# Kernel optimization log

Hardware: AMD Instinct MI355X
Metric: run time of the kernel (lower is better)

## Reference

```python
import jax, jax.numpy as jnp
import numpy as np

D_MODEL, D_INNER, D_STATE, DT_RANK, K = 768, 1536, 16, 48, 4
B, L = 2, 1024


def causal_depthwise_conv(x, w, b):
    # x: [B, L, D], w: [D, 1, K], b: [D]; torch pads K-1 both sides then slices [:L] -> causal left pad
    xt = x.transpose(0, 2, 1)  # [B, D, L]
    out = jax.lax.conv_general_dilated(
        xt, w, window_strides=(1,), padding=[(K - 1, 0)],
        dimension_numbers=('NCH', 'OIH', 'NCH'), feature_group_count=xt.shape[1])
    return out.transpose(0, 2, 1) + b


def ssm(xc, A_log, D, W_dt, dtW, dtb, W_B, W_C):
    # xc: [B, L, Din]
    A = -jnp.exp(A_log)                                   # [Din, N]
    dt_low = jnp.einsum('bld,rd->blr', xc, W_dt)          # [B, L, R]
    delta = jax.nn.softplus(jnp.einsum('blr,dr->bld', dt_low, dtW) + dtb)  # [B, L, Din]
    Bm = jnp.einsum('bld,nd->bln', xc, W_B)               # [B, L, N]
    Cm = jnp.einsum('bld,nd->bln', xc, W_C)               # [B, L, N]
    deltaA = jnp.exp(delta[..., None] * A)                # [B, L, Din, N]
    BX = (delta * xc)[..., None] * Bm[:, :, None, :]      # [B, L, Din, N]

    def combine(e1, e2):
        a1, b1 = e1
        a2, b2 = e2
        return a1 * a2, a2 * b1 + b2

    _, hs = jax.lax.associative_scan(combine, (deltaA, BX), axis=1)  # [B, L, Din, N]
    y = jnp.einsum('bldn,bln->bld', hs, Cm) + D * xc
    return y


def setup_inputs() -> dict:
    key = jax.random.key(0)
    ks = jax.random.split(key, 20)
    s = 0.02
    A_init = jnp.log(jnp.broadcast_to(jnp.arange(1, D_STATE + 1, dtype=jnp.float32), (D_INNER, D_STATE)))
    return {
        'x': jax.random.normal(ks[0], (B, L, D_MODEL), jnp.float32),
        'W_in_states': jax.random.normal(ks[1], (D_INNER, D_MODEL), jnp.float32) * s,
        'W_in_gates': jax.random.normal(ks[2], (D_INNER, D_MODEL), jnp.float32) * s,
        'conv_w': jax.random.normal(ks[3], (D_INNER, 1, K), jnp.float32) * 0.2,
        'conv_b': jax.random.normal(ks[4], (D_INNER,), jnp.float32) * 0.02,
        'conv_w_b': jax.random.normal(ks[5], (D_INNER, 1, K), jnp.float32) * 0.2,
        'conv_b_b': jax.random.normal(ks[6], (D_INNER,), jnp.float32) * 0.02,
        'W_dt': jax.random.normal(ks[7], (DT_RANK, D_INNER), jnp.float32) * s,
        'W_B': jax.random.normal(ks[8], (D_STATE, D_INNER), jnp.float32) * s,
        'W_C': jax.random.normal(ks[9], (D_STATE, D_INNER), jnp.float32) * s,
        'dtW': jax.random.normal(ks[10], (D_INNER, DT_RANK), jnp.float32) * s,
        'dtb': jax.random.normal(ks[11], (D_INNER,), jnp.float32) * 0.1,
        'A_log': A_init,
        'Dp': jnp.ones((D_INNER,), jnp.float32),
        'W_dt_b': jax.random.normal(ks[12], (DT_RANK, D_INNER), jnp.float32) * s,
        'W_B_b': jax.random.normal(ks[13], (D_STATE, D_INNER), jnp.float32) * s,
        'W_C_b': jax.random.normal(ks[14], (D_STATE, D_INNER), jnp.float32) * s,
        'dtW_b': jax.random.normal(ks[15], (D_INNER, DT_RANK), jnp.float32) * s,
        'dtb_b': jax.random.normal(ks[16], (D_INNER,), jnp.float32) * 0.1,
        'A_log_b': A_init,
        'Dp_b': jnp.ones((D_INNER,), jnp.float32),
        'W_out': jax.random.normal(ks[17], (D_MODEL, D_INNER), jnp.float32) * s,
    }


def reference(x, W_in_states, W_in_gates, conv_w, conv_b, conv_w_b, conv_b_b,
              W_dt, W_B, W_C, dtW, dtb, A_log, Dp,
              W_dt_b, W_B_b, W_C_b, dtW_b, dtb_b, A_log_b, Dp_b, W_out):
    xs = jnp.einsum('blm,dm->bld', x, W_in_states)  # [B, L, Din]
    z = jnp.einsum('blm,dm->bld', x, W_in_gates)    # [B, L, Din]
    # forward branch
    xc = jax.nn.silu(causal_depthwise_conv(xs, conv_w, conv_b))
    y = ssm(xc, A_log, Dp, W_dt, dtW, dtb, W_B, W_C)
    # backward branch: xz flipped along L, split -> reversed xs / reversed z
    xs_b = xs[:, ::-1]
    z_b = z[:, ::-1]
    xcb = jax.nn.silu(causal_depthwise_conv(xs_b, conv_w_b, conv_b_b))
    y_b = ssm(xcb, A_log_b, Dp_b, W_dt_b, dtW_b, dtb_b, W_B_b, W_C_b)
    # gating
    y = y * jax.nn.silu(z)
    y_b = y_b * jax.nn.silu(z_b)
    y = (y + y_b[:, ::-1]) * 0.5  # divide_output
    return jnp.einsum('bld,md->blm', y, W_out)
```

## Files before the change

### kernel.cpp

```cpp
#include <hip/hip_runtime.h>
#include <hip/hip_bf16.h>
#include <stdint.h>

#define DM 768
#define DI 1536
#define DSTATE 16
#define RNK 48
#define BB 2
#define LL 1024
#define ML (BB * LL)

#define NSEG 32
#define SEGL (LL / NSEG)

typedef unsigned short u16;
typedef __bf16 bf16x8 __attribute__((ext_vector_type(8)));
typedef float f32x4 __attribute__((ext_vector_type(4)));

struct __align__(8) u16x4_t { u16 x, y, z, w; };

__device__ __forceinline__ float b2f(u16 u) {
  union { uint32_t i; float f; } v; v.i = ((uint32_t)u) << 16; return v.f;
}
__device__ __forceinline__ u16 f2b(float f) {
  union { float f; uint32_t i; } v; v.f = f;
  uint32_t r = v.i + 0x7FFFu + ((v.i >> 16) & 1u);
  return (u16)(r >> 16);
}
__device__ __forceinline__ float silu_f(float x) { return x / (1.f + __expf(-x)); }
__device__ __forceinline__ float softplus_f(float s) {
  return fmaxf(s, 0.f) + __logf(1.f + __expf(-fabsf(s)));
}
__device__ __forceinline__ u16x4_t cvt4(float4 v) {
  u16x4_t o; o.x = f2b(v.x); o.y = f2b(v.y); o.z = f2b(v.z); o.w = f2b(v.w); return o;
}

#define SEG_X    (ML * DM / 4)
#define SEG_W    (DI * DM / 4)
#define SEG_CAT  (128 * DI / 4)
#define SEG_DTW  (DI * 64 / 4)
__global__ __launch_bounds__(256) void convert_kernel(
    const float4* __restrict__ x, const float4* __restrict__ wis,
    const float4* __restrict__ wig, const float4* __restrict__ wout,
    const float* __restrict__ W_B, const float* __restrict__ W_C,
    const float* __restrict__ W_dt,
    const float* __restrict__ W_B_b, const float* __restrict__ W_C_b,
    const float* __restrict__ W_dt_b,
    const float* __restrict__ dtW, const float* __restrict__ dtW_b,
    u16x4_t* __restrict__ xb, u16x4_t* __restrict__ wisb,
    u16x4_t* __restrict__ wigb, u16x4_t* __restrict__ woutb,
    u16x4_t* __restrict__ wcf, u16x4_t* __restrict__ wcb,
    u16x4_t* __restrict__ dtwf, u16x4_t* __restrict__ dtwb)
{
  int idx = blockIdx.x * 256 + threadIdx.x;
  if (idx < SEG_X) { xb[idx] = cvt4(x[idx]); return; }
  idx -= SEG_X;
  if (idx < SEG_W) { wisb[idx] = cvt4(wis[idx]); return; }
  idx -= SEG_W;
  if (idx < SEG_W) { wigb[idx] = cvt4(wig[idx]); return; }
  idx -= SEG_W;
  if (idx < SEG_W) { woutb[idx] = cvt4(wout[idx]); return; }
  idx -= SEG_W;
  if (idx < 2 * SEG_CAT) {
    int dir = idx / SEG_CAT;
    int rem = idx % SEG_CAT;
    int row = rem / (DI / 4), k4 = rem % (DI / 4);
    const float* src = nullptr;
    if (row < 16)      src = (dir ? W_B_b  : W_B)  + (size_t)row * DI + k4 * 4;
    else if (row < 32) src = (dir ? W_C_b  : W_C)  + (size_t)(row - 16) * DI + k4 * 4;
    else if (row < 80) src = (dir ? W_dt_b : W_dt) + (size_t)(row - 32) * DI + k4 * 4;
    u16x4_t o;
    if (src) o = cvt4(*(const float4*)src);
    else { o.x = 0; o.y = 0; o.z = 0; o.w = 0; }
    (dir ? wcb : wcf)[rem] = o;
    return;
  }
  idx -= 2 * SEG_CAT;
  int dir = idx / SEG_DTW;
  int rem = idx % SEG_DTW;
  int d = rem / 16, r4 = rem % 16;
  const float* Dw = dir ? dtW_b : dtW;
  u16x4_t o;
  if (r4 < 12) o = cvt4(*(const float4*)(Dw + (size_t)d * RNK + r4 * 4));
  else { o.x = 0; o.y = 0; o.z = 0; o.w = 0; }
  (dir ? dtwb : dtwf)[rem] = o;
}

__global__ __launch_bounds__(256) void gemm_bt(
    const u16* __restrict__ A, const u16* __restrict__ B0,
    const u16* __restrict__ B1, int Nsplit,
    void* __restrict__ Cout, int M, int N, int K, int ldc, int epi,
    const u16* __restrict__ A2, const u16* __restrict__ B2,
    void* __restrict__ C2,
    u16* __restrict__ Caux, u16* __restrict__ Caux2,
    const float* __restrict__ ebias, const float* __restrict__ ebias2)
{
  if (blockIdx.z) { A = A2; B0 = B2; Cout = C2; Caux = Caux2; ebias = ebias2; }
  __shared__ alignas(16) u16 As[128 * 32];
  __shared__ alignas(16) u16 Bs[128 * 32];
  const int tid = threadIdx.x;
  const int wave = tid >> 6, lane = tid & 63;
  const int bm = blockIdx.y * 128;
  const int bn = blockIdx.x * 128;

  const u16* Bmat = B0;
  int ncol0 = bn;
  int epi_l = epi;
  if (B1 != nullptr && bn >= Nsplit) { Bmat = B1; ncol0 = bn - Nsplit; epi_l = 1; }

  const int c0 = tid, c1 = tid + 256;
  const u16* gA0 = A + (size_t)(bm + (c0 >> 2)) * K + (c0 & 3) * 8;
  const u16* gA1 = A + (size_t)(bm + (c1 >> 2)) * K + (c1 & 3) * 8;
  const u16* gB0 = Bmat + (size_t)(ncol0 + (c0 >> 2)) * K + (c0 & 3) * 8;
  const u16* gB1 = Bmat + (size_t)(ncol0 + (c1 >> 2)) * K + (c1 & 3) * 8;
  uint4* lA0 = (uint4*)&As[c0 * 8]; uint4* lA1 = (uint4*)&As[c1 * 8];
  uint4* lB0 = (uint4*)&Bs[c0 * 8]; uint4* lB1 = (uint4*)&Bs[c1 * 8];

  const int wm = (wave & 1) * 64, wn = (wave >> 1) * 64;
  const int rl = lane & 15, q = lane >> 4;

  f32x4 acc[4][4];
#pragma unroll
  for (int i = 0; i < 4; ++i)
#pragma unroll
    for (int j = 0; j < 4; ++j) acc[i][j] = (f32x4){0.f, 0.f, 0.f, 0.f};

  const bf16x8* AsV = (const bf16x8*)As;
  const bf16x8* BsV = (const bf16x8*)Bs;

  uint4 ra0 = *(const uint4*)(gA0);
  uint4 ra1 = *(const uint4*)(gA1);
  uint4 rb0 = *(const uint4*)(gB0);
  uint4 rb1 = *(const uint4*)(gB1);

  for (int k0 = 0; k0 < K; k0 += 32) {
    *lA0 = ra0; *lA1 = ra1; *lB0 = rb0; *lB1 = rb1;
    __syncthreads();
    if (k0 + 32 < K) {
      ra0 = *(const uint4*)(gA0 + k0 + 32);
      ra1 = *(const uint4*)(gA1 + k0 + 32);
      rb0 = *(const uint4*)(gB0 + k0 + 32);
      rb1 = *(const uint4*)(gB1 + k0 + 32);
    }
    bf16x8 af[4], bfv[4];
#pragma unroll
    for (int s = 0; s < 4; ++s) {
      af[s]  = AsV[(wm + s * 16 + rl) * 4 + q];
      bfv[s] = BsV[(wn + s * 16 + rl) * 4 + q];
    }
#pragma unroll
    for (int i = 0; i < 4; ++i)
#pragma unroll
      for (int j = 0; j < 4; ++j)
        acc[i][j] = __builtin_amdgcn_mfma_f32_16x16x32_bf16(af[i], bfv[j], acc[i][j], 0, 0, 0);
    __syncthreads();
  }

#pragma unroll
  for (int i = 0; i < 4; ++i) {
#pragma unroll
    for (int j = 0; j < 4; ++j) {
#pragma unroll
      for (int r = 0; r < 4; ++r) {
        int row = bm + wm + i * 16 + q * 4 + r;
        int col = bn + wn + j * 16 + rl;
        float v = acc[i][j][r];
        if (epi_l == 1) v = silu_f(v);
        if (epi == 5) {
          if (col < 32)      ((float*)Cout)[(size_t)row * 32 + col] = v;
          else if (col < 96) Caux[(size_t)row * 64 + (col - 32)] = f2b(v);
        } else if (epi == 6) {
          ((u16*)Cout)[(size_t)row * ldc + col] = f2b(softplus_f(v + ebias[col]));
        } else if (epi == 2) {
          ((float*)Cout)[(size_t)row * ldc + col] = v;
        } else {
          ((u16*)Cout)[(size_t)row * ldc + col] = f2b(v);
        }
      }
    }
  }
}

__global__ __launch_bounds__(256) void gemm_out64(
    const u16* __restrict__ A, const u16* __restrict__ Bw,
    float* __restrict__ out)
{
  __shared__ alignas(16) u16 As[64 * 72];
  __shared__ alignas(16) u16 Bs[64 * 72];
  const int tid = threadIdx.x;
  const int wave = tid >> 6, lane = tid & 63;
  const int bm = blockIdx.y * 64;
  const int bn = blockIdx.x * 64;

  const int c0 = tid, c1 = tid + 256;
  const u16* gA0 = A + (size_t)(bm + (c0 >> 3)) * DI + (c0 & 7) * 8;
  const u16* gA1 = A + (size_t)(bm + (c1 >> 3)) * DI + (c1 & 7) * 8;
  const u16* gB0 = Bw + (size_t)(bn + (c0 >> 3)) * DI + (c0 & 7) * 8;
  const u16* gB1 = Bw + (size_t)(bn + (c1 >> 3)) * DI + (c1 & 7) * 8;
  uint4* lA0 = (uint4*)&As[(c0 >> 3) * 72 + (c0 & 7) * 8];
  uint4* lA1 = (uint4*)&As[(c1 >> 3) * 72 + (c1 & 7) * 8];
  uint4* lB0 = (uint4*)&Bs[(c0 >> 3) * 72 + (c0 & 7) * 8];
  uint4* lB1 = (uint4*)&Bs[(c1 >> 3) * 72 + (c1 & 7) * 8];

  const int rl = lane & 15, q = lane >> 4;

  f32x4 acc[4];
#pragma unroll
  for (int s = 0; s < 4; ++s) acc[s] = (f32x4){0.f, 0.f, 0.f, 0.f};

  uint4 ra0 = *(const uint4*)gA0, ra1 = *(const uint4*)gA1;
  uint4 rb0 = *(const uint4*)gB0, rb1 = *(const uint4*)gB1;

  for (int k0 = 0; k0 < DI; k0 += 64) {
    *lA0 = ra0; *lA1 = ra1; *lB0 = rb0; *lB1 = rb1;
    __syncthreads();
    if (k0 + 64 < DI) {
      ra0 = *(const uint4*)(gA0 + k0 + 64);
      ra1 = *(const uint4*)(gA1 + k0 + 64);
      rb0 = *(const uint4*)(gB0 + k0 + 64);
      rb1 = *(const uint4*)(gB1 + k0 + 64);
    }
    bf16x8 bf[2], af;
#pragma unroll
    for (int c = 0; c < 2; ++c)
      bf[c] = *(const bf16x8*)&Bs[(wave * 16 + rl) * 72 + c * 32 + q * 8];
#pragma unroll
    for (int s = 0; s < 4; ++s) {
#pragma unroll
      for (int c = 0; c < 2; ++c) {
        af = *(const bf16x8*)&As[(s * 16 + rl) * 72 + c * 32 + q * 8];
        acc[s] = __builtin_amdgcn_mfma_f32_16x16x32_bf16(af, bf[c], acc[s], 0, 0, 0);
      }
    }
    __syncthreads();
  }

#pragma unroll
  for (int s = 0; s < 4; ++s) {
#pragma unroll
    for (int r = 0; r < 4; ++r) {
      int row = bm + s * 16 + q * 4 + r;
      int col = bn + wave * 16 + rl;
      out[(size_t)row * DM + col] = acc[s][r];
    }
  }
}

__global__ void conv_kernel(
    const u16* __restrict__ xsg,
    const float* __restrict__ cw, const float* __restrict__ cb,
    const float* __restrict__ cwb, const float* __restrict__ cbb,
    u16* __restrict__ xc, u16* __restrict__ xcb)
{
  int idx = blockIdx.x * 256 + threadIdx.x;
  int d = idx % DI;
  int row = idx / DI;
  int l = row % LL, b = row / LL;
  const u16* base = xsg + (size_t)b * LL * 3072 + d;

  float4 wf = *(const float4*)(cw + d * 4);
  float4 wb = *(const float4*)(cwb + d * 4);
  float wfk[4] = {wf.x, wf.y, wf.z, wf.w};
  float wbk[4] = {wb.x, wb.y, wb.z, wb.w};

  float accf = cb[d];
  float accb = cbb[d];
#pragma unroll
  for (int k = 0; k < 4; ++k) {
    int ls = l - 3 + k;
    if (ls >= 0) {
      accf += wfk[k] * b2f(base[(size_t)ls * 3072]);
      accb += wbk[k] * b2f(base[(size_t)(LL - 1 - ls) * 3072]);
    }
  }
  xc[idx]  = f2b(silu_f(accf));
  xcb[idx] = f2b(silu_f(accb));
}

__global__ void combine_kernel(
    const u16* __restrict__ ybr, const u16* __restrict__ xsg, u16* yf)
{
  int idx = blockIdx.x * 256 + threadIdx.x;
  int d = idx % DI;
  int row = idx / DI;
  int l = row % LL, b = row / LL;
  float g = b2f(xsg[(size_t)row * 3072 + DI + d]);
  float vb = b2f(ybr[((size_t)b * LL + (LL - 1 - l)) * DI + d]);
  float v = 0.5f * (b2f(yf[idx]) + vb) * g;
  yf[idx] = f2b(v);
}

__global__ __launch_bounds__(256) void scan_sum(
    const u16* __restrict__ df, const u16* __restrict__ db,
    const u16* __restrict__ xcf, const u16* __restrict__ xcb,
    const float* __restrict__ pf, const float* __restrict__ pb,
    const float* __restrict__ A_log, const float* __restrict__ A_log_b,
    float* __restrict__ sdl, float* __restrict__ bs)
{
  const int dir = blockIdx.z / NSEG, seg = blockIdx.z % NSEG;
  const u16* delta = dir ? db : df;
  const u16* xc = dir ? xcb : xcf;
  const float* proj = dir ? pb : pf;
  const float* Al = dir ? A_log_b : A_log;
  const int b = blockIdx.y;
  const int d = blockIdx.x * 256 + threadIdx.x;
  const int l0 = seg * SEGL;

  __shared__ float Bsh[SEGL][16];
  for (int i = threadIdx.x; i < SEGL * 16; i += 256) {
    int l = i >> 4, n = i & 15;
    Bsh[l][n] = proj[((size_t)b * LL + l0 + l) * 32 + n];
  }
  __syncthreads();

  float An[16];
#pragma unroll
  for (int n = 0; n < 16; ++n) An[n] = -__expf(Al[d * 16 + n]);

  float h[16];
#pragma unroll
  for (int n = 0; n < 16; ++n) h[n] = 0.f;
  float S = 0.f;

  const u16* dbase = delta + ((size_t)b * LL + l0) * DI + d;
  const u16* xbase = xc + ((size_t)b * LL + l0) * DI + d;

  for (int g = 0; g < SEGL; g += 4) {
    float dl4[4], dx4[4];
#pragma unroll
    for (int j = 0; j < 4; ++j) {
      float dv = b2f(dbase[(size_t)(g + j) * DI]);
      float xv = b2f(xbase[(size_t)(g + j) * DI]);
      dl4[j] = dv; dx4[j] = dv * xv;
    }
#pragma unroll
    for (int j = 0; j < 4; ++j) {
      S += dl4[j];
#pragma unroll
      for (int n = 0; n < 16; ++n)
        h[n] = __expf(dl4[j] * An[n]) * h[n] + dx4[j] * Bsh[g + j][n];
    }
  }

  size_t base = (((size_t)dir * BB + b) * NSEG + seg) * DI + d;
  sdl[base] = S;
#pragma unroll
  for (int n = 0; n < 16; ++n) bs[base * 16 + n] = h[n];
}

__global__ __launch_bounds__(256) void scan_carry(
    const float* __restrict__ A_log, const float* __restrict__ A_log_b,
    const float* __restrict__ sdl, float* __restrict__ bs)
{
  int idx = blockIdx.x * 256 + threadIdx.x;
  int n = idx & 15;
  int t = idx >> 4;
  int d = t % DI;
  int b = (t / DI) % BB;
  int dir = t / (DI * BB);
  const float* Al = dir ? A_log_b : A_log;
  float An = -__expf(Al[d * 16 + n]);
  float h = 0.f;
  for (int s = 0; s < NSEG; ++s) {
    size_t base = (((size_t)dir * BB + b) * NSEG + s) * DI + d;
    float S = sdl[base];
    float bv = bs[base * 16 + n];
    bs[base * 16 + n] = h;
    h = __expf(S * An) * h + bv;
  }
}

__global__ __launch_bounds__(256) void scan_apply(
    const u16* __restrict__ df, const u16* __restrict__ db,
    const u16* __restrict__ xcf, const u16* __restrict__ xcb,
    const float* __restrict__ pf, const float* __restrict__ pb,
    const float* __restrict__ A_log, const float* __restrict__ A_log_b,
    const float* __restrict__ Dp, const float* __restrict__ Dp_b,
    const float* __restrict__ bs,
    u16* __restrict__ y_f, u16* __restrict__ y_b)
{
  const int dir = blockIdx.z / NSEG, seg = blockIdx.z % NSEG;
  const u16* delta = dir ? db : df;
  const u16* xc = dir ? xcb : xcf;
  const float* proj = dir ? pb : pf;
  const float* Al = dir ? A_log_b : A_log;
  const float* Dpp = dir ? Dp_b : Dp;
  u16* y = dir ? y_b : y_f;
  const int b = blockIdx.y;
  const int d = blockIdx.x * 256 + threadIdx.x;
  const int l0 = seg * SEGL;

  __shared__ float BCsh[SEGL][32];
  for (int i = threadIdx.x; i < SEGL * 32; i += 256) {
    int l = i >> 5, j = i & 31;
    BCsh[l][j] = proj[((size_t)b * LL + l0 + l) * 32 + j];
  }
  __syncthreads();

  float An[16];
#pragma unroll
  for (int n = 0; n < 16; ++n) An[n] = -__expf(Al[d * 16 + n]);
  const float Dv = Dpp[d];

  float h[16];
  size_t cbase = (((size_t)dir * BB + b) * NSEG + seg) * DI + d;
#pragma unroll
  for (int n = 0; n < 16; ++n) h[n] = bs[cbase * 16 + n];

  const u16* dbase = delta + ((size_t)b * LL + l0) * DI + d;
  const u16* xbase = xc + ((size_t)b * LL + l0) * DI + d;
  u16* ybase = y + ((size_t)b * LL + l0) * DI + d;

  for (int g = 0; g < SEGL; g += 4) {
    float dl4[4], xv4[4];
#pragma unroll
    for (int j = 0; j < 4; ++j) {
      dl4[j] = b2f(dbase[(size_t)(g + j) * DI]);
      xv4[j] = b2f(xbase[(size_t)(g + j) * DI]);
    }
#pragma unroll
    for (int j = 0; j < 4; ++j) {
      float dx = dl4[j] * xv4[j];
      float yv = 0.f;
#pragma unroll
      for (int n = 0; n < 16; ++n) {
        h[n] = __expf(dl4[j] * An[n]) * h[n] + dx * BCsh[g + j][n];
        yv += h[n] * BCsh[g + j][16 + n];
      }
      ybase[(size_t)(g + j) * DI] = f2b(yv + Dv * xv4[j]);
    }
  }
}

extern "C" void kernel_launch(void* const* d_in, const int* in_sizes, int n_in,
                              void* d_out, int out_size, void* d_ws, size_t ws_size,
                              hipStream_t stream)
{
  const float* x       = (const float*)d_in[0];
  const float* Wis     = (const float*)d_in[1];
  const float* Wig     = (const float*)d_in[2];
  const float* conv_w  = (const float*)d_in[3];
  const float* conv_b  = (const float*)d_in[4];
  const float* conv_wb = (const float*)d_in[5];
  const float* conv_bb = (const float*)d_in[6];
  const float* W_dt    = (const float*)d_in[7];
  const float* W_B     = (const float*)d_in[8];
  const float* W_C     = (const float*)d_in[9];
  const float* dtW     = (const float*)d_in[10];
  const float* dtb     = (const float*)d_in[11];
  const float* A_log   = (const float*)d_in[12];
  const float* Dp      = (const float*)d_in[13];
  const float* W_dt_b  = (const float*)d_in[14];
  const float* W_B_b   = (const float*)d_in[15];
  const float* W_C_b   = (const float*)d_in[16];
  const float* dtW_b   = (const float*)d_in[17];
  const float* dtb_b   = (const float*)d_in[18];
  const float* A_log_b = (const float*)d_in[19];
  const float* Dp_b    = (const float*)d_in[20];
  const float* W_out   = (const float*)d_in[21];

  char* ws = (char*)d_ws;
  size_t off = 0;
  auto alloc = [&](size_t bytes) -> char* {
    char* p = ws + off; off += (bytes + 255) & ~(size_t)255; return p;
  };
  u16*   xb    = (u16*)alloc((size_t)ML * DM * 2);
  u16*   wisb  = (u16*)alloc((size_t)DI * DM * 2);
  u16*   wigb  = (u16*)alloc((size_t)DI * DM * 2);
  u16*   woutb = (u16*)alloc((size_t)DM * DI * 2);
  u16*   xsg = (u16*)alloc((size_t)ML * 3072 * 2);
  u16*   xc  = (u16*)alloc((size_t)ML * DI * 2);
  u16*   xcb = (u16*)alloc((size_t)ML * DI * 2);
  u16*   wcf = (u16*)alloc((size_t)128 * DI * 2);
  u16*   wcb = (u16*)alloc((size_t)128 * DI * 2);
  u16*   dtwf = (u16*)alloc((size_t)DI * 64 * 2);
  u16*   dtwb = (u16*)alloc((size_t)DI * 64 * 2);
  float* pf  = (float*)alloc((size_t)ML * 32 * 4);
  float* pb  = (float*)alloc((size_t)ML * 32 * 4);
  u16*   dtlf = (u16*)alloc((size_t)ML * 64 * 2);
  u16*   dtlb = (u16*)alloc((size_t)ML * 64 * 2);
  u16*   df  = (u16*)alloc((size_t)ML * DI * 2);
  u16*   db  = (u16*)alloc((size_t)ML * DI * 2);
  u16*   yf  = (u16*)alloc((size_t)ML * DI * 2);
  u16*   ybr = (u16*)alloc((size_t)ML * DI * 2);
  float* sdl = (float*)alloc((size_t)2 * BB * NSEG * DI * 4);
  float* bs  = (float*)alloc((size_t)2 * BB * NSEG * DI * 16 * 4);

  const int conv_total = SEG_X + 3 * SEG_W + 2 * SEG_CAT + 2 * SEG_DTW;
  convert_kernel<<<(conv_total + 255) / 256, 256, 0, stream>>>(
      (const float4*)x, (const float4*)Wis, (const float4*)Wig, (const float4*)W_out,
      W_B, W_C, W_dt, W_B_b, W_C_b, W_dt_b, dtW, dtW_b,
      (u16x4_t*)xb, (u16x4_t*)wisb, (u16x4_t*)wigb, (u16x4_t*)woutb,
      (u16x4_t*)wcf, (u16x4_t*)wcb, (u16x4_t*)dtwf, (u16x4_t*)dtwb);

  gemm_bt<<<dim3(3072 / 128, ML / 128, 1), 256, 0, stream>>>(
      xb, wisb, wigb, DI, xsg, ML, 3072, DM, 3072, 0,
      nullptr, nullptr, nullptr, nullptr, nullptr, nullptr, nullptr);

  conv_kernel<<<(ML * DI) / 256, 256, 0, stream>>>(
      xsg, conv_w, conv_b, conv_wb, conv_bb, xc, xcb);

  gemm_bt<<<dim3(1, ML / 128, 2), 256, 0, stream>>>(
      xc, wcf, nullptr, 1 << 30, pf, ML, 128, DI, 32, 5,
      xcb, wcb, pb, dtlf, dtlb, nullptr, nullptr);

  gemm_bt<<<dim3(DI / 128, ML / 128, 2), 256, 0, stream>>>(
      dtlf, dtwf, nullptr, 1 << 30, df, ML, DI, 64, DI, 6,
      dtlb, dtwb, db, nullptr, nullptr, dtb, dtb_b);

  scan_sum<<<dim3(DI / 256, BB, 2 * NSEG), 256, 0, stream>>>(
      df, db, xc, xcb, pf, pb, A_log, A_log_b, sdl, bs);
  scan_carry<<<(2 * BB * DI * 16) / 256, 256, 0, stream>>>(
      A_log, A_log_b, sdl, bs);
  scan_apply<<<dim3(DI / 256, BB, 2 * NSEG), 256, 0, stream>>>(
      df, db, xc, xcb, pf, pb, A_log, A_log_b, Dp, Dp_b, bs, yf, ybr);

  combine_kernel<<<(ML * DI) / 256, 256, 0, stream>>>(ybr, xsg, yf);

  gemm_out64<<<dim3(DM / 64, ML / 64, 1), 256, 0, stream>>>(
      yf, woutb, (float*)d_out);
}
```

Measured before the change: 285.5 us.

## Double-buffer GEMM LDS tiles using direct global-to-LDS loads

The bf16 MFMA GEMM now stages A/B tiles with global_load_lds, writing straight into LDS and skipping the register round-trip. LDS is split into two buffers so the next K-slice loads while the current one is consumed. This cuts the loop to one barrier per iteration instead of two. It doubles LDS use per block and relies on the barrier waiting for the async LDS-DMA writes to complete.

```diff
diff --git a/kernel.cpp b/kernel.cpp
--- a/kernel.cpp
+++ b/kernel.cpp
@@ -33,6 +33,12 @@
 }
 __device__ __forceinline__ u16x4_t cvt4(float4 v) {
   u16x4_t o; o.x = f2b(v.x); o.y = f2b(v.y); o.z = f2b(v.z); o.w = f2b(v.w); return o;
+}
+
+__device__ __forceinline__ void gl16(const u16* g, u16* l) {
+  __builtin_amdgcn_global_load_lds(
+      (const __attribute__((address_space(1))) uint32_t*)g,
+      (__attribute__((address_space(3))) uint32_t*)l, 16, 0, 0);
 }
 
 #define SEG_X    (ML * DM / 4)
@@ -96,8 +102,8 @@
     const float* __restrict__ ebias, const float* __restrict__ ebias2)
 {
   if (blockIdx.z) { A = A2; B0 = B2; Cout = C2; Caux = Caux2; ebias = ebias2; }
-  __shared__ alignas(16) u16 As[128 * 32];
-  __shared__ alignas(16) u16 Bs[128 * 32];
+  __shared__ alignas(16) u16 As[2][128 * 32];
+  __shared__ alignas(16) u16 Bs[2][128 * 32];
   const int tid = threadIdx.x;
   const int wave = tid >> 6, lane = tid & 63;
   const int bm = blockIdx.y * 128;
@@ -113,8 +119,6 @@
   const u16* gA1 = A + (size_t)(bm + (c1 >> 2)) * K + (c1 & 3) * 8;
   const u16* gB0 = Bmat + (size_t)(ncol0 + (c0 >> 2)) * K + (c0 & 3) * 8;
   const u16* gB1 = Bmat + (size_t)(ncol0 + (c1 >> 2)) * K + (c1 & 3) * 8;
-  uint4* lA0 = (uint4*)&As[c0 * 8]; uint4* lA1 = (uint4*)&As[c1 * 8];
-  uint4* lB0 = (uint4*)&Bs[c0 * 8]; uint4* lB1 = (uint4*)&Bs[c1 * 8];
 
   const int wm = (wave & 1) * 64, wn = (wave >> 1) * 64;
   const int rl = lane & 15, q = lane >> 4;
@@ -125,23 +129,22 @@
 #pragma unroll
     for (int j = 0; j < 4; ++j) acc[i][j] = (f32x4){0.f, 0.f, 0.f, 0.f};
 
-  const bf16x8* AsV = (const bf16x8*)As;
-  const bf16x8* BsV = (const bf16x8*)Bs;
-
-  uint4 ra0 = *(const uint4*)(gA0);
-  uint4 ra1 = *(const uint4*)(gA1);
-  uint4 rb0 = *(const uint4*)(gB0);
-  uint4 rb1 = *(const uint4*)(gB1);
-
+  auto stage = [&](int buf, int k0) {
+    gl16(gA0 + k0, &As[buf][c0 * 8]);
+    gl16(gA1 + k0, &As[buf][c1 * 8]);
+    gl16(gB0 + k0, &Bs[buf][c0 * 8]);
+    gl16(gB1 + k0, &Bs[buf][c1 * 8]);
+  };
+
+  stage(0, 0);
+  __syncthreads();
+  int cur = 0;
   for (int k0 = 0; k0 < K; k0 += 32) {
-    *lA0 = ra0; *lA1 = ra1; *lB0 = rb0; *lB1 = rb1;
-    __syncthreads();
-    if (k0 + 32 < K) {
-      ra0 = *(const uint4*)(gA0 + k0 + 32);
-      ra1 = *(const uint4*)(gA1 + k0 + 32);
-      rb0 = *(const uint4*)(gB0 + k0 + 32);
-      rb1 = *(const uint4*)(gB1 + k0 + 32);
-    }
+    const bool more = (k0 + 32 < K);
+    if (more) stage(cur ^ 1, k0 + 32);
+
+    const bf16x8* AsV = (const bf16x8*)As[cur];
+    const bf16x8* BsV = (const bf16x8*)Bs[cur];
     bf16x8 af[4], bfv[4];
 #pragma unroll
     for (int s = 0; s < 4; ++s) {
@@ -153,7 +156,11 @@
 #pragma unroll
       for (int j = 0; j < 4; ++j)
         acc[i][j] = __builtin_amdgcn_mfma_f32_16x16x32_bf16(af[i], bfv[j], acc[i][j], 0, 0, 0);
-    __syncthreads();
+
+    if (more) {
+      __syncthreads();
+      cur ^= 1;
+    }
   }
 
 #pragma unroll
```

New measurement: 305.5 us. 7.0% more time.
